# Kernel tuning notes

Hardware: AMD Instinct MI355X
Metric: run time of the kernel (lower is better)

The kernel has to match this reference:

```python
import jax, jax.numpy as jnp
import numpy as np

N_USERS = 100000
N_ITEMS = 100000
D_FEAT = 256
BATCH = 8192
CLASSES = 5
E = 500000
D_CONV = 128
D_RAW = 256
D_EMB = 256
NUM_BASIS = 2
BN_EPS = 1e-3  # tf.contrib.layers.batch_norm default epsilon


def _bn_params(key, dim):
    # packed [gamma, beta, moving_mean, moving_var]
    return jnp.stack([jnp.ones(dim), jnp.zeros(dim), jnp.zeros(dim), jnp.ones(dim)]).astype(jnp.float32)


def setup_inputs() -> dict:
    key = jax.random.key(0)
    ks = jax.random.split(key, 24)
    s = lambda fan_in, fan_out: np.sqrt(2.0 / (fan_in + fan_out)).astype(np.float32)
    inp = {
        'user_feat': jax.random.normal(ks[0], (N_USERS, D_FEAT), jnp.float32),
        'item_feat': jax.random.normal(ks[1], (N_ITEMS, D_FEAT), jnp.float32),
        'user_idx': jax.random.randint(ks[2], (BATCH,), 0, N_USERS, jnp.int32),
        'item_idx': jax.random.randint(ks[3], (BATCH,), 0, N_ITEMS, jnp.int32),
        'user_edge_src': jax.random.randint(ks[4], (CLASSES, E), 0, N_ITEMS, jnp.int32),
        'user_edge_dst': jax.random.randint(ks[5], (CLASSES, E), 0, BATCH, jnp.int32),
        'user_edge_w': jax.random.uniform(ks[6], (CLASSES, E), jnp.float32),
        'item_edge_src': jax.random.randint(ks[7], (CLASSES, E), 0, N_USERS, jnp.int32),
        'item_edge_dst': jax.random.randint(ks[8], (CLASSES, E), 0, BATCH, jnp.int32),
        'item_edge_w': jax.random.uniform(ks[9], (CLASSES, E), jnp.float32),
        'W_fu': jax.random.normal(ks[10], (D_FEAT, D_RAW), jnp.float32) * s(D_FEAT, D_RAW),
        'b_fu': jnp.zeros((D_RAW,), jnp.float32),
        'W_fi': jax.random.normal(ks[11], (D_FEAT, D_RAW), jnp.float32) * s(D_FEAT, D_RAW),
        'b_fi': jnp.zeros((D_RAW,), jnp.float32),
        'W_uc': jax.random.normal(ks[12], (CLASSES, D_FEAT, D_CONV), jnp.float32) * s(D_FEAT, D_CONV),
        'W_ic': jax.random.normal(ks[13], (CLASSES, D_FEAT, D_CONV), jnp.float32) * s(D_FEAT, D_CONV),
        'bn_fu': _bn_params(ks[14], D_RAW),
        'bn_hu': _bn_params(ks[15], CLASSES * D_CONV),
        'bn_fi': _bn_params(ks[16], D_RAW),
        'bn_hi': _bn_params(ks[17], CLASSES * D_CONV),
        'W2_fu': jax.random.normal(ks[18], (D_RAW, D_EMB), jnp.float32) * s(D_RAW, D_EMB),
        'W2_hu': jax.random.normal(ks[19], (CLASSES * D_CONV, D_EMB), jnp.float32) * s(CLASSES * D_CONV, D_EMB),
        'W2_fi': jax.random.normal(ks[20], (D_RAW, D_EMB), jnp.float32) * s(D_RAW, D_EMB),
        'W2_hi': jax.random.normal(ks[21], (CLASSES * D_CONV, D_EMB), jnp.float32) * s(CLASSES * D_CONV, D_EMB),
        'Wdec': jax.random.normal(ks[22], (NUM_BASIS, D_EMB, D_EMB), jnp.float32) * s(D_EMB, D_EMB),
        'Wcomb': jax.random.normal(ks[23], (CLASSES, NUM_BASIS), jnp.float32) * s(CLASSES, NUM_BASIS),
    }
    return inp


def _bn(x, p):
    gamma, beta, mean, var = p[0], p[1], p[2], p[3]
    return gamma * (x - mean) * jax.lax.rsqrt(var + BN_EPS) + beta


def _agg(feat, src, dst, w, n_rows):
    # weighted sparse [B, N] x dense [N, D] aggregation via gather + segment_sum
    msgs = feat[src] * w[:, None]  # [E, D]
    return jax.ops.segment_sum(msgs, dst, num_segments=n_rows)


def reference(user_feat, item_feat, user_idx, item_idx,
              user_edge_src, user_edge_dst, user_edge_w,
              item_edge_src, item_edge_dst, item_edge_w,
              W_fu, b_fu, W_fi, b_fi, W_uc, W_ic,
              bn_fu, bn_hu, bn_fi, bn_hi,
              W2_fu, W2_hu, W2_fi, W2_hi, Wdec, Wcomb):
    B = user_idx.shape[0]
    classes = W_uc.shape[0]

    # batch row selection (sparse.matmul with one-hot selector == gather)
    f_user = user_feat[user_idx] @ W_fu + b_fu  # [B, D_RAW]
    f_item = item_feat[item_idx] @ W_fi + b_fi

    # per-class graph convolution: aggregate opposite-side features, project, stack
    h_user = jnp.concatenate(
        [_agg(item_feat, user_edge_src[c], user_edge_dst[c], user_edge_w[c], B) @ W_uc[c]
         for c in range(classes)], axis=1)  # [B, classes*D_CONV]
    h_item = jnp.concatenate(
        [_agg(user_feat, item_edge_src[c], item_edge_dst[c], item_edge_w[c], B) @ W_ic[c]
         for c in range(classes)], axis=1)

    # batchnorm (inference stats) + relu  (dropout rate 0 -> identity)
    f_user = jax.nn.relu(_bn(f_user, bn_fu))
    f_item = jax.nn.relu(_bn(f_item, bn_fi))
    h_user = jax.nn.relu(_bn(h_user, bn_hu))
    h_item = jax.nn.relu(_bn(h_item, bn_hi))

    user_emb = jax.nn.relu(f_user @ W2_fu + h_user @ W2_hu)  # [B, D_EMB]
    item_emb = jax.nn.relu(f_item @ W2_fi + h_item @ W2_hi)

    # bilinear decoder: per-class kernel = sum_k Wcomb[r,k] * Wdec[k]
    kernels = jnp.einsum('rk,kij->rij', Wcomb, Wdec)  # [classes, D_EMB, D_EMB]
    logits = jnp.einsum('bi,rij,bj->br', user_emb, kernels, item_emb)  # [B, classes]
    return logits


if __name__ == '__main__':
    out = reference(**setup_inputs())
    print(out.shape, out.dtype)
```

## Files before the change

kernel.cpp:

```cpp
#include <hip/hip_runtime.h>
#include <cstdint>
#include <cstddef>

#define NBATCH   8192
#define DFEAT    256
#define DCONV    128
#define NCLASS   5
#define NEDGE    500000
#define NUSERS   100000
#define BN_EPS   1e-3f
#define NBUCKET  128
#define BROWS    64
#define CAP      4608
#define NPHB     16
#define NPHU     13

typedef unsigned short u16;
typedef short bf16x8_t __attribute__((ext_vector_type(8)));
typedef float f32x4_t  __attribute__((ext_vector_type(4)));

__device__ __forceinline__ u16 f2bf(float x) {
    unsigned u = __float_as_uint(x);
    u += 0x7FFF + ((u >> 16) & 1);
    return (u16)(u >> 16);
}
__device__ __forceinline__ float bf2f(u16 h) {
    return __uint_as_float(((unsigned)h) << 16);
}

template<int AF32>
__device__ __forceinline__ void mfma_tiles_t(
    const void* __restrict__ Av, int lda, const int* __restrict__ gather,
    const u16* __restrict__ BT, int K,
    int tileM, int tileN, u16* As, u16* Bs, f32x4_t acc[4])
{
    const int t    = threadIdx.x;
    const int rowi = t >> 2;
    const int kc   = t & 3;
    const int w    = t >> 6;
    const int lane = t & 63;

    int ar = gather ? gather[tileM + rowi] : (tileM + rowi);
    const u16*   Ap16 = (const u16*)Av   + (size_t)ar * lda + kc * 8;
    const float* Apf  = (const float*)Av + (size_t)ar * lda + kc * 8;
    const u16* Bp = BT + (size_t)(tileN + rowi) * K + kc * 8;
    u16* Aw = As + (size_t)(((rowi >> 4) * 64) + (rowi & 15) + 16 * kc) * 8;
    u16* Bw = Bs + (size_t)(((rowi >> 4) * 64) + (rowi & 15) + 16 * kc) * 8;
    const u16* Ar = As + (size_t)(w * 64 + lane) * 8;

    for (int k0 = 0; k0 < K; k0 += 32) {
        __syncthreads();
        if (AF32) {
            float4 a0 = *(const float4*)(Apf + k0);
            float4 a1 = *(const float4*)(Apf + k0 + 4);
            ushort4 p0, p1;
            p0.x = f2bf(a0.x); p0.y = f2bf(a0.y); p0.z = f2bf(a0.z); p0.w = f2bf(a0.w);
            p1.x = f2bf(a1.x); p1.y = f2bf(a1.y); p1.z = f2bf(a1.z); p1.w = f2bf(a1.w);
            *(ushort4*)Aw = p0;
            *(ushort4*)(Aw + 4) = p1;
        } else {
            *(uint4*)Aw = *(const uint4*)(Ap16 + k0);
        }
        *(uint4*)Bw = *(const uint4*)(Bp + k0);
        __syncthreads();
        bf16x8_t av = *(const bf16x8_t*)Ar;
        #pragma unroll
        for (int nb = 0; nb < 4; ++nb) {
            bf16x8_t bv = *(const bf16x8_t*)(Bs + (size_t)(nb * 64 + lane) * 8);
            acc[nb] = __builtin_amdgcn_mfma_f32_16x16x32_bf16(av, bv, acc[nb], 0, 0, 0);
        }
    }
}

__device__ __forceinline__ void epilogue(
    f32x4_t acc[4], int tileM, int tileN,
    const float* __restrict__ bias, const float* __restrict__ bn, int bn_ld,
    int relu, u16* __restrict__ out_bf, float* __restrict__ out_f32, int ldc)
{
    const int t = threadIdx.x, w = t >> 6, lane = t & 63;
    const int row0 = tileM + w * 16 + (lane >> 4) * 4;
    #pragma unroll
    for (int nb = 0; nb < 4; ++nb) {
        int col = tileN + nb * 16 + (lane & 15);
        float g = 1.f, be = 0.f, mu = 0.f, va = 1.f, bs = 0.f;
        if (bn)   { g = bn[col]; be = bn[bn_ld + col]; mu = bn[2 * bn_ld + col]; va = bn[3 * bn_ld + col]; }
        if (bias) bs = bias[col];
        #pragma unroll
        for (int r = 0; r < 4; ++r) {
            float x = acc[nb][r] + bs;
            if (bn)   x = g * (x - mu) * rsqrtf(va + BN_EPS) + be;
            if (relu) x = fmaxf(x, 0.f);
            size_t o = (size_t)(row0 + r) * ldc + col;
            if (out_bf) out_bf[o] = f2bf(x);
            else        out_f32[o] = x;
        }
    }
}

__global__ __launch_bounds__(256) void k_gemm_f(
    const float* __restrict__ uf, const float* __restrict__ itf,
    const int* __restrict__ uidx, const int* __restrict__ iidx,
    const u16* __restrict__ WTu, const u16* __restrict__ WTi,
    const float* __restrict__ bu, const float* __restrict__ bi,
    const float* __restrict__ bnu, const float* __restrict__ bni,
    u16* __restrict__ outu, u16* __restrict__ outi)
{
    __shared__ __align__(16) u16 As[2048], Bs[2048];
    f32x4_t z4 = {0.f, 0.f, 0.f, 0.f};
    f32x4_t acc[4] = {z4, z4, z4, z4};
    int z = blockIdx.z;
    const float* feat = z ? itf : uf;
    const int* idx  = z ? iidx : uidx;
    const u16* WT   = z ? WTi : WTu;
    const float* bias = z ? bi : bu;
    const float* bn   = z ? bni : bnu;
    u16* out = z ? outi : outu;
    int tileM = blockIdx.x * 64, tileN = blockIdx.y * 64;
    mfma_tiles_t<1>(feat, 256, idx, WT, 256, tileM, tileN, As, Bs, acc);
    epilogue(acc, tileM, tileN, bias, bn, 256, 1, out, nullptr, 256);
}

__global__ __launch_bounds__(256) void k_hproj(
    const u16* __restrict__ agg, const u16* __restrict__ WucT, const u16* __restrict__ WicT,
    const float* __restrict__ bn_hu, const float* __restrict__ bn_hi,
    u16* __restrict__ h_user, u16* __restrict__ h_item)
{
    __shared__ __align__(16) u16 As[2048], Bs[2048];
    f32x4_t z4 = {0.f, 0.f, 0.f, 0.f};
    f32x4_t acc[4] = {z4, z4, z4, z4};
    int cs = blockIdx.z, c = cs % NCLASS, side = cs / NCLASS;
    const u16* A  = agg + (size_t)cs * NBATCH * DFEAT;
    const u16* BT = (side ? WicT : WucT) + (size_t)c * DCONV * DFEAT;
    const float* bn = (side ? bn_hi : bn_hu) + c * DCONV;
    u16* out = (side ? h_item : h_user) + c * DCONV;
    int tileM = blockIdx.x * 64, tileN = blockIdx.y * 64;
    mfma_tiles_t<0>(A, 256, nullptr, BT, 256, tileM, tileN, As, Bs, acc);
    epilogue(acc, tileM, tileN, nullptr, bn, NCLASS * DCONV, 1, out, nullptr, NCLASS * DCONV);
}

__global__ __launch_bounds__(256) void k_emb(
    const u16* __restrict__ fu, const u16* __restrict__ fi,
    const u16* __restrict__ hu, const u16* __restrict__ hi,
    const u16* __restrict__ W2fTu, const u16* __restrict__ W2hTu,
    const u16* __restrict__ W2fTi, const u16* __restrict__ W2hTi,
    u16* __restrict__ embu, u16* __restrict__ embi)
{
    __shared__ __align__(16) u16 As[2048], Bs[2048];
    f32x4_t z4 = {0.f, 0.f, 0.f, 0.f};
    f32x4_t acc[4] = {z4, z4, z4, z4};
    int z = blockIdx.z;
    const u16* fbf  = z ? fi : fu;
    const u16* hbf  = z ? hi : hu;
    const u16* W2fT = z ? W2fTi : W2fTu;
    const u16* W2hT = z ? W2hTi : W2hTu;
    u16* emb = z ? embi : embu;
    int tileM = blockIdx.x * 64, tileN = blockIdx.y * 64;
    mfma_tiles_t<0>(fbf, 256, nullptr, W2fT, 256, tileM, tileN, As, Bs, acc);
    mfma_tiles_t<0>(hbf, NCLASS * DCONV, nullptr, W2hT, NCLASS * DCONV, tileM, tileN, As, Bs, acc);
    epilogue(acc, tileM, tileN, nullptr, nullptr, 0, 1, emb, nullptr, 256);
}

__global__ __launch_bounds__(256) void k_dec(
    const u16* __restrict__ emb, const u16* __restrict__ WdecT,
    float* __restrict__ t0, float* __restrict__ t1)
{
    __shared__ __align__(16) u16 As[2048], Bs[2048];
    f32x4_t z4 = {0.f, 0.f, 0.f, 0.f};
    f32x4_t acc[4] = {z4, z4, z4, z4};
    int zi = blockIdx.z;
    const u16* BT = WdecT + (size_t)zi * 256 * 256;
    float* out = zi ? t1 : t0;
    int tileM = blockIdx.x * 64, tileN = blockIdx.y * 64;
    mfma_tiles_t<0>(emb, 256, nullptr, BT, 256, tileM, tileN, As, Bs, acc);
    epilogue(acc, tileM, tileN, nullptr, nullptr, 0, 0, nullptr, out, 256);
}

__global__ __launch_bounds__(256) void cvt_feat(
    const float* __restrict__ uf, const float* __restrict__ itf,
    u16* __restrict__ ubf, u16* __restrict__ ibf)
{
    const size_t n4 = (size_t)NUSERS * DFEAT / 4;
    for (size_t i = (size_t)blockIdx.x * 256 + threadIdx.x; i < 2 * n4;
         i += (size_t)gridDim.x * 256) {
        bool u = i < n4;
        size_t j = u ? i : i - n4;
        float4 v = u ? ((const float4*)uf)[j] : ((const float4*)itf)[j];
        ushort4 o;
        o.x = f2bf(v.x); o.y = f2bf(v.y); o.z = f2bf(v.z); o.w = f2bf(v.w);
        ((ushort4*)(u ? ubf : ibf))[j] = o;
    }
}

#define OFF_WFU   0
#define OFF_WFI   65536
#define OFF_WUC   131072
#define OFF_WIC   294912
#define OFF_W2FU  458752
#define OFF_W2HU  524288
#define OFF_W2FI  688128
#define OFF_W2HI  753664
#define OFF_WDEC  917504

__global__ __launch_bounds__(256) void cvt_wt(
    const float* __restrict__ Wfu, const float* __restrict__ Wfi,
    const float* __restrict__ Wuc, const float* __restrict__ Wic,
    const float* __restrict__ W2fu, const float* __restrict__ W2hu,
    const float* __restrict__ W2fi, const float* __restrict__ W2hi,
    const float* __restrict__ Wdec, u16* __restrict__ wT)
{
    __shared__ float tile[32][33];
    const float* in; u16* out; int K, N, B;
    switch (blockIdx.y) {
        case 0: in = Wfu;  out = wT + OFF_WFU;  K = 256; N = 256; B = 1; break;
        case 1: in = Wfi;  out = wT + OFF_WFI;  K = 256; N = 256; B = 1; break;
        case 2: in = Wuc;  out = wT + OFF_WUC;  K = 256; N = 128; B = 5; break;
        case 3: in = Wic;  out = wT + OFF_WIC;  K = 256; N = 128; B = 5; break;
        case 4: in = W2fu; out = wT + OFF_W2FU; K = 256; N = 256; B = 1; break;
        case 5: in = W2hu; out = wT + OFF_W2HU; K = 640; N = 256; B = 1; break;
        case 6: in = W2fi; out = wT + OFF_W2FI; K = 256; N = 256; B = 1; break;
        case 7: in = W2hi; out = wT + OFF_W2HI; K = 640; N = 256; B = 1; break;
        default: in = Wdec; out = wT + OFF_WDEC; K = 256; N = 256; B = 2; break;
    }
    int tk = K >> 5, tn = N >> 5;
    int tid = blockIdx.x;
    if (tid >= B * tk * tn) return;
    int b  = tid / (tk * tn);
    int r  = tid - b * tk * tn;
    int kt = r % tk, nt = r / tk;
    int k0 = kt * 32, n0 = nt * 32;
    int ty = threadIdx.x >> 5, tx = threadIdx.x & 31;
    const float* ip = in + (size_t)b * K * N;
    u16* op = out + (size_t)b * N * K;
    #pragma unroll
    for (int i = 0; i < 4; ++i) {
        int row = ty + 8 * i;
        tile[row][tx] = ip[(size_t)(k0 + row) * N + (n0 + tx)];
    }
    __syncthreads();
    #pragma unroll
    for (int i = 0; i < 4; ++i) {
        int row = ty + 8 * i;
        op[(size_t)(n0 + row) * K + (k0 + tx)] = f2bf(tile[tx][row]);
    }
}

__global__ __launch_bounds__(256) void init_bcur(int* __restrict__ bcur)
{
    int i = blockIdx.x * 256 + threadIdx.x;
    if (i < 10 * NBUCKET) bcur[i] = (i & (NBUCKET - 1)) * CAP;
}

__global__ __launch_bounds__(256) void partition_kernel(
    const int* __restrict__ u_src, const int* __restrict__ u_dst, const float* __restrict__ u_w,
    const int* __restrict__ i_src, const int* __restrict__ i_dst, const float* __restrict__ i_w,
    int* __restrict__ bcur, uint2* __restrict__ part)
{
    __shared__ int hist[NBUCKET];
    __shared__ int cur[NBUCKET];
    int cs = blockIdx.y;
    const int* srcp; const int* dstp; const float* wp;
    if (cs < NCLASS) {
        srcp = u_src + (size_t)cs * NEDGE;
        dstp = u_dst + (size_t)cs * NEDGE;
        wp   = u_w   + (size_t)cs * NEDGE;
    } else {
        int c = cs - NCLASS;
        srcp = i_src + (size_t)c * NEDGE;
        dstp = i_dst + (size_t)c * NEDGE;
        wp   = i_w   + (size_t)c * NEDGE;
    }
    int lo_e = (int)(((long long)blockIdx.x * NEDGE) / gridDim.x);
    int hi_e = (int)(((long long)(blockIdx.x + 1) * NEDGE) / gridDim.x);

    for (int i = threadIdx.x; i < NBUCKET; i += 256) hist[i] = 0;
    __syncthreads();
    for (int e = lo_e + threadIdx.x; e < hi_e; e += 256)
        atomicAdd(&hist[dstp[e] >> 6], 1);
    __syncthreads();
    for (int i = threadIdx.x; i < NBUCKET; i += 256)
        cur[i] = atomicAdd(&bcur[cs * NBUCKET + i], hist[i]);
    __syncthreads();
    uint2* out = part + (size_t)cs * NBUCKET * CAP;
    for (int e = lo_e + threadIdx.x; e < hi_e; e += 256) {
        int dst = dstp[e];
        int bkt = dst >> 6;
        int pos = atomicAdd(&cur[bkt], 1);
        if (pos < bkt * CAP + CAP)
            out[pos] = make_uint2((unsigned)srcp[e] | ((unsigned)(dst & 63) << 24),
                                  __float_as_uint(wp[e]));
    }
}

__device__ __forceinline__ int edge_key(unsigned x) {
    return (int)((x >> 24) * NPHB) + (int)((x & 0xFFFFFFu) >> 13);
}

__global__ __launch_bounds__(512) void spmm_sorted(
    const u16* __restrict__ item_bf, const u16* __restrict__ user_bf,
    const uint2* __restrict__ part, const int* __restrict__ bcur,
    u16* __restrict__ agg)
{
    __shared__ int bin_cnt[BROWS * NPHB];
    __shared__ int bin_off[BROWS * NPHB + 1];
    __shared__ int bin_cur[BROWS * NPHB];
    __shared__ int wsum[8];
    __shared__ __align__(8) uint2 sorted[CAP];
    int id   = blockIdx.x;
    int side = id & 1;
    int k    = id >> 1;
    int c    = k >> 7;
    int b    = k & 127;
    int cs   = side * NCLASS + c;
    const u16* feat = side ? user_bf : item_bf;
    int n = bcur[cs * NBUCKET + b] - b * CAP;
    if (n > CAP) n = CAP;
    const uint2* ew = part + ((size_t)cs * NBUCKET + b) * CAP;
    int tid = threadIdx.x, wave = tid >> 6, lane = tid & 63;

    bin_cnt[tid] = 0;
    bin_cnt[tid + 512] = 0;
    __syncthreads();
    for (int e = tid; e < n; e += 512)
        atomicAdd(&bin_cnt[edge_key(ew[e].x)], 1);
    __syncthreads();
    {
        int i2 = tid * 2;
        int c0 = bin_cnt[i2], c1 = bin_cnt[i2 + 1];
        int s = c0 + c1;
        int v = s;
        #pragma unroll
        for (int o = 1; o < 64; o <<= 1) {
            int u = __shfl_up(v, o);
            if (lane >= o) v += u;
        }
        if (lane == 63) wsum[wave] = v;
        __syncthreads();
        if (tid < 8) {
            int s8 = wsum[tid];
            #pragma unroll
            for (int o = 1; o < 8; o <<= 1) {
                int u = __shfl_up(s8, o);
                if (lane >= o) s8 += u;
            }
            wsum[tid] = s8;
        }
        __syncthreads();
        int base = (wave ? wsum[wave - 1] : 0) + (v - s);
        bin_off[i2] = base;
        bin_off[i2 + 1] = base + c0;
        bin_cur[i2] = base;
        bin_cur[i2 + 1] = base + c0;
        if (tid == 511) bin_off[1024] = base + s;
    }
    __syncthreads();
    for (int e = tid; e < n; e += 512) {
        uint2 p = ew[e];
        int pos = atomicAdd(&bin_cur[edge_key(p.x)], 1);
        sorted[pos] = p;
    }
    __syncthreads();

    int rowbase = cs * NBATCH + b * BROWS;
    float ax[8], ay[8], az[8], aw[8];
    #pragma unroll
    for (int r0 = 0; r0 < 8; ++r0) { ax[r0] = 0.f; ay[r0] = 0.f; az[r0] = 0.f; aw[r0] = 0.f; }

    for (int ph = 0; ph < NPHU; ++ph) {
        #pragma unroll
        for (int r0 = 0; r0 < 8; ++r0) {
            int bi = (wave * 8 + r0) * NPHB + ph;
            int j0 = bin_off[bi], j1 = bin_off[bi + 1];
            int j = j0;
            for (; j + 7 < j1; j += 8) {
                uint2 p[8];
                #pragma unroll
                for (int q = 0; q < 8; ++q) p[q] = sorted[j + q];
                ushort4 v[8];
                #pragma unroll
                for (int q = 0; q < 8; ++q)
                    v[q] = *(const ushort4*)&feat[(size_t)(p[q].x & 0xFFFFFF) * DFEAT + lane * 4];
                #pragma unroll
                for (int q = 0; q < 8; ++q) {
                    float w = __uint_as_float(p[q].y);
                    ax[r0] += w * bf2f(v[q].x);
                    ay[r0] += w * bf2f(v[q].y);
                    az[r0] += w * bf2f(v[q].z);
                    aw[r0] += w * bf2f(v[q].w);
                }
            }
            for (; j + 3 < j1; j += 4) {
                uint2 p0 = sorted[j], p1 = sorted[j + 1], p2 = sorted[j + 2], p3 = sorted[j + 3];
                ushort4 v0 = *(const ushort4*)&feat[(size_t)(p0.x & 0xFFFFFF) * DFEAT + lane * 4];
                ushort4 v1 = *(const ushort4*)&feat[(size_t)(p1.x & 0xFFFFFF) * DFEAT + lane * 4];
                ushort4 v2 = *(const ushort4*)&feat[(size_t)(p2.x & 0xFFFFFF) * DFEAT + lane * 4];
                ushort4 v3 = *(const ushort4*)&feat[(size_t)(p3.x & 0xFFFFFF) * DFEAT + lane * 4];
                float w0 = __uint_as_float(p0.y), w1 = __uint_as_float(p1.y);
                float w2 = __uint_as_float(p2.y), w3 = __uint_as_float(p3.y);
                ax[r0] += w0 * bf2f(v0.x) + w1 * bf2f(v1.x) + w2 * bf2f(v2.x) + w3 * bf2f(v3.x);
                ay[r0] += w0 * bf2f(v0.y) + w1 * bf2f(v1.y) + w2 * bf2f(v2.y) + w3 * bf2f(v3.y);
                az[r0] += w0 * bf2f(v0.z) + w1 * bf2f(v1.z) + w2 * bf2f(v2.z) + w3 * bf2f(v3.z);
                aw[r0] += w0 * bf2f(v0.w) + w1 * bf2f(v1.w) + w2 * bf2f(v2.w) + w3 * bf2f(v3.w);
            }
            for (; j < j1; ++j) {
                uint2 p0 = sorted[j];
                ushort4 v0 = *(const ushort4*)&feat[(size_t)(p0.x & 0xFFFFFF) * DFEAT + lane * 4];
                float w0 = __uint_as_float(p0.y);
                ax[r0] += w0 * bf2f(v0.x);
                ay[r0] += w0 * bf2f(v0.y);
                az[r0] += w0 * bf2f(v0.z);
                aw[r0] += w0 * bf2f(v0.w);
            }
        }
    }

    #pragma unroll
    for (int r0 = 0; r0 < 8; ++r0) {
        ushort4 o4;
        o4.x = f2bf(ax[r0]); o4.y = f2bf(ay[r0]); o4.z = f2bf(az[r0]); o4.w = f2bf(aw[r0]);
        *(ushort4*)&agg[(size_t)(rowbase + wave * 8 + r0) * 256 + lane * 4] = o4;
    }
}

__global__ __launch_bounds__(256) void decoder_kernel(
    const float* __restrict__ t0, const float* __restrict__ t1,
    const u16* __restrict__ item_emb, const float* __restrict__ Wcomb,
    float* __restrict__ out)
{
    int wave = threadIdx.x >> 6;
    int lane = threadIdx.x & 63;
    int b = blockIdx.x * 4 + wave;
    const u16*   ie = item_emb + (size_t)b * 256;
    const float* p0 = t0 + (size_t)b * 256;
    const float* p1 = t1 + (size_t)b * 256;
    float s0 = 0.f, s1 = 0.f;
    #pragma unroll
    for (int j = lane; j < 256; j += 64) {
        float v = bf2f(ie[j]);
        s0 += p0[j] * v;
        s1 += p1[j] * v;
    }
    #pragma unroll
    for (int o = 32; o > 0; o >>= 1) {
        s0 += __shfl_down(s0, o);
        s1 += __shfl_down(s1, o);
    }
    if (lane == 0) {
        #pragma unroll
        for (int r = 0; r < NCLASS; ++r)
            out[b * NCLASS + r] = Wcomb[r * 2 + 0] * s0 + Wcomb[r * 2 + 1] * s1;
    }
}

extern "C" void kernel_launch(void* const* d_in, const int* in_sizes, int n_in,
                              void* d_out, int out_size, void* d_ws, size_t ws_size,
                              hipStream_t stream)
{
    const float* user_feat = (const float*)d_in[0];
    const float* item_feat = (const float*)d_in[1];
    const int*   user_idx  = (const int*)  d_in[2];
    const int*   item_idx  = (const int*)  d_in[3];
    const int*   u_src     = (const int*)  d_in[4];
    const int*   u_dst     = (const int*)  d_in[5];
    const float* u_w       = (const float*)d_in[6];
    const int*   i_src     = (const int*)  d_in[7];
    const int*   i_dst     = (const int*)  d_in[8];
    const float* i_w       = (const float*)d_in[9];
    const float* W_fu      = (const float*)d_in[10];
    const float* b_fu      = (const float*)d_in[11];
    const float* W_fi      = (const float*)d_in[12];
    const float* b_fi      = (const float*)d_in[13];
    const float* W_uc      = (const float*)d_in[14];
    const float* W_ic      = (const float*)d_in[15];
    const float* bn_fu     = (const float*)d_in[16];
    const float* bn_hu     = (const float*)d_in[17];
    const float* bn_fi     = (const float*)d_in[18];
    const float* bn_hi     = (const float*)d_in[19];
    const float* W2_fu     = (const float*)d_in[20];
    const float* W2_hu     = (const float*)d_in[21];
    const float* W2_fi     = (const float*)d_in[22];
    const float* W2_hi     = (const float*)d_in[23];
    const float* Wdec      = (const float*)d_in[24];
    const float* Wcomb     = (const float*)d_in[25];
    float* out = (float*)d_out;

    char* ws = (char*)d_ws;
    int*   bcur       = (int*)  (ws + 0);
    uint2* part_ew    = (uint2*)(ws + 65536);
    u16*   user_bf    = (u16*)  (ws + 47251456);
    u16*   item_bf    = (u16*)  (ws + 98451456);
    u16*   agg_bf     = (u16*)  (ws + 149651456);
    u16*   wT         = (u16*)  (ws + 191594496);
    u16*   f_user_bf  = (u16*)  (ws + 65536);
    u16*   f_item_bf  = (u16*)  (ws + 4259840);
    u16*   h_user_bf  = (u16*)  (ws + 8454144);
    u16*   h_item_bf  = (u16*)  (ws + 18939904);
    float* t0         = (float*)(ws + 149651456);
    float* t1         = (float*)(ws + 158040064);
    u16*   user_emb   = (u16*)  (ws + 166428672);
    u16*   item_emb   = (u16*)  (ws + 170622976);

    init_bcur<<<5, 256, 0, stream>>>(bcur);
    partition_kernel<<<dim3(128, 10), 256, 0, stream>>>(
        u_src, u_dst, u_w, i_src, i_dst, i_w, bcur, part_ew);

    cvt_feat<<<4096, 256, 0, stream>>>(user_feat, item_feat, user_bf, item_bf);
    cvt_wt<<<dim3(160, 9), 256, 0, stream>>>(W_fu, W_fi, W_uc, W_ic,
                                             W2_fu, W2_hu, W2_fi, W2_hi, Wdec, wT);

    spmm_sorted<<<dim3(2 * NCLASS * NBUCKET), 512, 0, stream>>>(
        item_bf, user_bf, part_ew, bcur, agg_bf);

    k_gemm_f<<<dim3(128, 4, 2), 256, 0, stream>>>(
        user_feat, item_feat, user_idx, item_idx, wT + OFF_WFU, wT + OFF_WFI,
        b_fu, b_fi, bn_fu, bn_fi, f_user_bf, f_item_bf);

    k_hproj<<<dim3(128, 2, 10), 256, 0, stream>>>(agg_bf, wT + OFF_WUC, wT + OFF_WIC,
                                                  bn_hu, bn_hi, h_user_bf, h_item_bf);

    k_emb<<<dim3(128, 4, 2), 256, 0, stream>>>(
        f_user_bf, f_item_bf, h_user_bf, h_item_bf,
        wT + OFF_W2FU, wT + OFF_W2HU, wT + OFF_W2FI, wT + OFF_W2HI,
        user_emb, item_emb);

    k_dec<<<dim3(128, 4, 2), 256, 0, stream>>>(user_emb, wT + OFF_WDEC, t0, t1);
    decoder_kernel<<<NBATCH / 4, 256, 0, stream>>>(t0, t1, item_emb, Wcomb, out);
}
```

Measured before the change: 710.2 us.

## Merge prep kernels and feature/hidden GEMMs into single launches; flatten spmm phase loop

```diff
diff --git a/kernel.cpp b/kernel.cpp
--- a/kernel.cpp
+++ b/kernel.cpp
@@ -97,45 +97,48 @@
     }
 }
 
-__global__ __launch_bounds__(256) void k_gemm_f(
+__global__ __launch_bounds__(256) void k_fh(
     const float* __restrict__ uf, const float* __restrict__ itf,
     const int* __restrict__ uidx, const int* __restrict__ iidx,
     const u16* __restrict__ WTu, const u16* __restrict__ WTi,
     const float* __restrict__ bu, const float* __restrict__ bi,
     const float* __restrict__ bnu, const float* __restrict__ bni,
-    u16* __restrict__ outu, u16* __restrict__ outi)
+    u16* __restrict__ outu, u16* __restrict__ outi,
+    const u16* __restrict__ agg, const u16* __restrict__ WucT, const u16* __restrict__ WicT,
+    const float* __restrict__ bn_hu, const float* __restrict__ bn_hi,
+    u16* __restrict__ h_user, u16* __restrict__ h_item)
 {
     __shared__ __align__(16) u16 As[2048], Bs[2048];
     f32x4_t z4 = {0.f, 0.f, 0.f, 0.f};
     f32x4_t acc[4] = {z4, z4, z4, z4};
-    int z = blockIdx.z;
-    const float* feat = z ? itf : uf;
-    const int* idx  = z ? iidx : uidx;
-    const u16* WT   = z ? WTi : WTu;
-    const float* bias = z ? bi : bu;
-    const float* bn   = z ? bni : bnu;
-    u16* out = z ? outi : outu;
-    int tileM = blockIdx.x * 64, tileN = blockIdx.y * 64;
-    mfma_tiles_t<1>(feat, 256, idx, WT, 256, tileM, tileN, As, Bs, acc);
-    epilogue(acc, tileM, tileN, bias, bn, 256, 1, out, nullptr, 256);
-}
-
-__global__ __launch_bounds__(256) void k_hproj(
-    const u16* __restrict__ agg, const u16* __restrict__ WucT, const u16* __restrict__ WicT,
-    const float* __restrict__ bn_hu, const float* __restrict__ bn_hi,
-    u16* __restrict__ h_user, u16* __restrict__ h_item)
-{
-    __shared__ __align__(16) u16 As[2048], Bs[2048];
-    f32x4_t z4 = {0.f, 0.f, 0.f, 0.f};
-    f32x4_t acc[4] = {z4, z4, z4, z4};
-    int cs = blockIdx.z, c = cs % NCLASS, side = cs / NCLASS;
-    const u16* A  = agg + (size_t)cs * NBATCH * DFEAT;
-    const u16* BT = (side ? WicT : WucT) + (size_t)c * DCONV * DFEAT;
-    const float* bn = (side ? bn_hi : bn_hu) + c * DCONV;
-    u16* out = (side ? h_item : h_user) + c * DCONV;
-    int tileM = blockIdx.x * 64, tileN = blockIdx.y * 64;
-    mfma_tiles_t<0>(A, 256, nullptr, BT, 256, tileM, tileN, As, Bs, acc);
-    epilogue(acc, tileM, tileN, nullptr, bn, NCLASS * DCONV, 1, out, nullptr, NCLASS * DCONV);
+    int id = blockIdx.x;
+    if (id < 1024) {
+        int z  = id >> 9;
+        int ny = (id >> 7) & 3;
+        int mx = id & 127;
+        const float* feat = z ? itf : uf;
+        const int* idx  = z ? iidx : uidx;
+        const u16* WT   = z ? WTi : WTu;
+        const float* bias = z ? bi : bu;
+        const float* bn   = z ? bni : bnu;
+        u16* out = z ? outi : outu;
+        int tileM = mx * 64, tileN = ny * 64;
+        mfma_tiles_t<1>(feat, 256, idx, WT, 256, tileM, tileN, As, Bs, acc);
+        epilogue(acc, tileM, tileN, bias, bn, 256, 1, out, nullptr, 256);
+    } else {
+        int r  = id - 1024;
+        int cs = r >> 8;
+        int ny = (r >> 7) & 1;
+        int mx = r & 127;
+        int c = cs % NCLASS, side = cs / NCLASS;
+        const u16* A  = agg + (size_t)cs * NBATCH * DFEAT;
+        const u16* BT = (side ? WicT : WucT) + (size_t)c * DCONV * DFEAT;
+        const float* bn = (side ? bn_hi : bn_hu) + c * DCONV;
+        u16* out = (side ? h_item : h_user) + c * DCONV;
+        int tileM = mx * 64, tileN = ny * 64;
+        mfma_tiles_t<0>(A, 256, nullptr, BT, 256, tileM, tileN, As, Bs, acc);
+        epilogue(acc, tileM, tileN, nullptr, bn, NCLASS * DCONV, 1, out, nullptr, NCLASS * DCONV);
+    }
 }
 
 __global__ __launch_bounds__(256) void k_emb(
@@ -175,22 +178,6 @@
     epilogue(acc, tileM, tileN, nullptr, nullptr, 0, 0, nullptr, out, 256);
 }
 
-__global__ __launch_bounds__(256) void cvt_feat(
-    const float* __restrict__ uf, const float* __restrict__ itf,
-    u16* __restrict__ ubf, u16* __restrict__ ibf)
-{
-    const size_t n4 = (size_t)NUSERS * DFEAT / 4;
-    for (size_t i = (size_t)blockIdx.x * 256 + threadIdx.x; i < 2 * n4;
-         i += (size_t)gridDim.x * 256) {
-        bool u = i < n4;
-        size_t j = u ? i : i - n4;
-        float4 v = u ? ((const float4*)uf)[j] : ((const float4*)itf)[j];
-        ushort4 o;
-        o.x = f2bf(v.x); o.y = f2bf(v.y); o.z = f2bf(v.z); o.w = f2bf(v.w);
-        ((ushort4*)(u ? ubf : ibf))[j] = o;
-    }
-}
-
 #define OFF_WFU   0
 #define OFF_WFI   65536
 #define OFF_WUC   131072
@@ -201,46 +188,105 @@
 #define OFF_W2HI  753664
 #define OFF_WDEC  917504
 
-__global__ __launch_bounds__(256) void cvt_wt(
+__global__ __launch_bounds__(256) void prep_all(
+    const int* __restrict__ u_src, const int* __restrict__ u_dst, const float* __restrict__ u_w,
+    const int* __restrict__ i_src, const int* __restrict__ i_dst, const float* __restrict__ i_w,
+    int* __restrict__ bcur, uint2* __restrict__ part,
+    const float* __restrict__ uf, const float* __restrict__ itf,
+    u16* __restrict__ ubf, u16* __restrict__ ibf,
     const float* __restrict__ Wfu, const float* __restrict__ Wfi,
     const float* __restrict__ Wuc, const float* __restrict__ Wic,
     const float* __restrict__ W2fu, const float* __restrict__ W2hu,
     const float* __restrict__ W2fi, const float* __restrict__ W2hi,
     const float* __restrict__ Wdec, u16* __restrict__ wT)
 {
-    __shared__ float tile[32][33];
-    const float* in; u16* out; int K, N, B;
-    switch (blockIdx.y) {
-        case 0: in = Wfu;  out = wT + OFF_WFU;  K = 256; N = 256; B = 1; break;
-        case 1: in = Wfi;  out = wT + OFF_WFI;  K = 256; N = 256; B = 1; break;
-        case 2: in = Wuc;  out = wT + OFF_WUC;  K = 256; N = 128; B = 5; break;
-        case 3: in = Wic;  out = wT + OFF_WIC;  K = 256; N = 128; B = 5; break;
-        case 4: in = W2fu; out = wT + OFF_W2FU; K = 256; N = 256; B = 1; break;
-        case 5: in = W2hu; out = wT + OFF_W2HU; K = 640; N = 256; B = 1; break;
-        case 6: in = W2fi; out = wT + OFF_W2FI; K = 256; N = 256; B = 1; break;
-        case 7: in = W2hi; out = wT + OFF_W2HI; K = 640; N = 256; B = 1; break;
-        default: in = Wdec; out = wT + OFF_WDEC; K = 256; N = 256; B = 2; break;
-    }
-    int tk = K >> 5, tn = N >> 5;
-    int tid = blockIdx.x;
-    if (tid >= B * tk * tn) return;
-    int b  = tid / (tk * tn);
-    int r  = tid - b * tk * tn;
-    int kt = r % tk, nt = r / tk;
-    int k0 = kt * 32, n0 = nt * 32;
-    int ty = threadIdx.x >> 5, tx = threadIdx.x & 31;
-    const float* ip = in + (size_t)b * K * N;
-    u16* op = out + (size_t)b * N * K;
-    #pragma unroll
-    for (int i = 0; i < 4; ++i) {
-        int row = ty + 8 * i;
-        tile[row][tx] = ip[(size_t)(k0 + row) * N + (n0 + tx)];
-    }
-    __syncthreads();
-    #pragma unroll
-    for (int i = 0; i < 4; ++i) {
-        int row = ty + 8 * i;
-        op[(size_t)(n0 + row) * K + (k0 + tx)] = f2bf(tile[tx][row]);
+    __shared__ union {
+        struct { int hist[NBUCKET]; int cur[NBUCKET]; } p;
+        float tile[32][33];
+    } sm;
+    int id = blockIdx.x;
+    if (id < 1280) {
+        int cs = id / 128;
+        int bx = id - cs * 128;
+        const int* srcp; const int* dstp; const float* wp;
+        if (cs < NCLASS) {
+            srcp = u_src + (size_t)cs * NEDGE;
+            dstp = u_dst + (size_t)cs * NEDGE;
+            wp   = u_w   + (size_t)cs * NEDGE;
+        } else {
+            int c = cs - NCLASS;
+            srcp = i_src + (size_t)c * NEDGE;
+            dstp = i_dst + (size_t)c * NEDGE;
+            wp   = i_w   + (size_t)c * NEDGE;
+        }
+        int lo_e = (int)(((long long)bx * NEDGE) >> 7);
+        int hi_e = (int)(((long long)(bx + 1) * NEDGE) >> 7);
+
+        for (int i = threadIdx.x; i < NBUCKET; i += 256) sm.p.hist[i] = 0;
+        __syncthreads();
+        for (int e = lo_e + threadIdx.x; e < hi_e; e += 256)
+            atomicAdd(&sm.p.hist[dstp[e] >> 6], 1);
+        __syncthreads();
+        for (int i = threadIdx.x; i < NBUCKET; i += 256)
+            sm.p.cur[i] = atomicAdd(&bcur[cs * NBUCKET + i], sm.p.hist[i]);
+        __syncthreads();
+        uint2* out = part + (size_t)cs * NBUCKET * CAP;
+        for (int e = lo_e + threadIdx.x; e < hi_e; e += 256) {
+            int dst = dstp[e];
+            int bkt = dst >> 6;
+            int pos = atomicAdd(&sm.p.cur[bkt], 1);
+            if (pos < bkt * CAP + CAP)
+                out[pos] = make_uint2((unsigned)srcp[e] | ((unsigned)(dst & 63) << 24),
+                                      __float_as_uint(wp[e]));
+        }
+    } else if (id < 1280 + 4096) {
+        int bx = id - 1280;
+        const size_t n4 = (size_t)NUSERS * DFEAT / 4;
+        for (size_t i = (size_t)bx * 256 + threadIdx.x; i < 2 * n4;
+             i += (size_t)4096 * 256) {
+            bool u = i < n4;
+            size_t j = u ? i : i - n4;
+            float4 v = u ? ((const float4*)uf)[j] : ((const float4*)itf)[j];
+            ushort4 o;
+            o.x = f2bf(v.x); o.y = f2bf(v.y); o.z = f2bf(v.z); o.w = f2bf(v.w);
+            ((ushort4*)(u ? ubf : ibf))[j] = o;
+        }
+    } else {
+        int r0 = id - (1280 + 4096);
+        int cse = r0 / 160;
+        int tid = r0 - cse * 160;
+        const float* in; u16* out; int K, N, B;
+        switch (cse) {
+            case 0: in = Wfu;  out = wT + OFF_WFU;  K = 256; N = 256; B = 1; break;
+            case 1: in = Wfi;  out = wT + OFF_WFI;  K = 256; N = 256; B = 1; break;
+            case 2: in = Wuc;  out = wT + OFF_WUC;  K = 256; N = 128; B = 5; break;
+            case 3: in = Wic;  out = wT + OFF_WIC;  K = 256; N = 128; B = 5; break;
+            case 4: in = W2fu; out = wT + OFF_W2FU; K = 256; N = 256; B = 1; break;
+            case 5: in = W2hu; out = wT + OFF_W2HU; K = 640; N = 256; B = 1; break;
+            case 6: in = W2fi; out = wT + OFF_W2FI; K = 256; N = 256; B = 1; break;
+            case 7: in = W2hi; out = wT + OFF_W2HI; K = 640; N = 256; B = 1; break;
+            default: in = Wdec; out = wT + OFF_WDEC; K = 256; N = 256; B = 2; break;
+        }
+        int tk = K >> 5, tn = N >> 5;
+        if (tid >= B * tk * tn) return;
+        int b  = tid / (tk * tn);
+        int r  = tid - b * tk * tn;
+        int kt = r % tk, nt = r / tk;
+        int k0 = kt * 32, n0 = nt * 32;
+        int ty = threadIdx.x >> 5, tx = threadIdx.x & 31;
+        const float* ip = in + (size_t)b * K * N;
+        u16* op = out + (size_t)b * N * K;
+        #pragma unroll
+        for (int i = 0; i < 4; ++i) {
+            int row = ty + 8 * i;
+            sm.tile[row][tx] = ip[(size_t)(k0 + row) * N + (n0 + tx)];
+        }
+        __syncthreads();
+        #pragma unroll
+        for (int i = 0; i < 4; ++i) {
+            int row = ty + 8 * i;
+            op[(size_t)(n0 + row) * K + (k0 + tx)] = f2bf(sm.tile[tx][row]);
+        }
     }
 }
 
@@ -248,47 +294,6 @@
 {
     int i = blockIdx.x * 256 + threadIdx.x;
     if (i < 10 * NBUCKET) bcur[i] = (i & (NBUCKET - 1)) * CAP;
-}
-
-__global__ __launch_bounds__(256) void partition_kernel(
-    const int* __restrict__ u_src, const int* __restrict__ u_dst, const float* __restrict__ u_w,
-    const int* __restrict__ i_src, const int* __restrict__ i_dst, const float* __restrict__ i_w,
-    int* __restrict__ bcur, uint2* __restrict__ part)
-{
-    __shared__ int hist[NBUCKET];
-    __shared__ int cur[NBUCKET];
-    int cs = blockIdx.y;
-    const int* srcp; const int* dstp; const float* wp;
-    if (cs < NCLASS) {
-        srcp = u_src + (size_t)cs * NEDGE;
-        dstp = u_dst + (size_t)cs * NEDGE;
-        wp   = u_w   + (size_t)cs * NEDGE;
-    } else {
-        int c = cs - NCLASS;
-        srcp = i_src + (size_t)c * NEDGE;
-        dstp = i_dst + (size_t)c * NEDGE;
-        wp   = i_w   + (size_t)c * NEDGE;
-    }
-    int lo_e = (int)(((long long)blockIdx.x * NEDGE) / gridDim.x);
-    int hi_e = (int)(((long long)(blockIdx.x + 1) * NEDGE) / gridDim.x);
-
-    for (int i = threadIdx.x; i < NBUCKET; i += 256) hist[i] = 0;
-    __syncthreads();
-    for (int e = lo_e + threadIdx.x; e < hi_e; e += 256)
-        atomicAdd(&hist[dstp[e] >> 6], 1);
-    __syncthreads();
-    for (int i = threadIdx.x; i < NBUCKET; i += 256)
-        cur[i] = atomicAdd(&bcur[cs * NBUCKET + i], hist[i]);
-    __syncthreads();
-    uint2* out = part + (size_t)cs * NBUCKET * CAP;
-    for (int e = lo_e + threadIdx.x; e < hi_e; e += 256) {
-        int dst = dstp[e];
-        int bkt = dst >> 6;
-        int pos = atomicAdd(&cur[bkt], 1);
-        if (pos < bkt * CAP + CAP)
-            out[pos] = make_uint2((unsigned)srcp[e] | ((unsigned)(dst & 63) << 24),
-                                  __float_as_uint(wp[e]));
-    }
 }
 
 __device__ __forceinline__ int edge_key(unsigned x) {
@@ -365,51 +370,49 @@
     #pragma unroll
     for (int r0 = 0; r0 < 8; ++r0) { ax[r0] = 0.f; ay[r0] = 0.f; az[r0] = 0.f; aw[r0] = 0.f; }
 
-    for (int ph = 0; ph < NPHU; ++ph) {
-        #pragma unroll
-        for (int r0 = 0; r0 < 8; ++r0) {
-            int bi = (wave * 8 + r0) * NPHB + ph;
-            int j0 = bin_off[bi], j1 = bin_off[bi + 1];
-            int j = j0;
-            for (; j + 7 < j1; j += 8) {
-                uint2 p[8];
-                #pragma unroll
-                for (int q = 0; q < 8; ++q) p[q] = sorted[j + q];
-                ushort4 v[8];
-                #pragma unroll
-                for (int q = 0; q < 8; ++q)
-                    v[q] = *(const ushort4*)&feat[(size_t)(p[q].x & 0xFFFFFF) * DFEAT + lane * 4];
-                #pragma unroll
-                for (int q = 0; q < 8; ++q) {
-                    float w = __uint_as_float(p[q].y);
-                    ax[r0] += w * bf2f(v[q].x);
-                    ay[r0] += w * bf2f(v[q].y);
-                    az[r0] += w * bf2f(v[q].z);
-                    aw[r0] += w * bf2f(v[q].w);
-                }
+    #pragma unroll
+    for (int r0 = 0; r0 < 8; ++r0) {
+        int base = (wave * 8 + r0) * NPHB;
+        int j0 = bin_off[base], j1 = bin_off[base + NPHU];
+        int j = j0;
+        for (; j + 7 < j1; j += 8) {
+            uint2 p[8];
+            #pragma unroll
+            for (int q = 0; q < 8; ++q) p[q] = sorted[j + q];
+            ushort4 v[8];
+            #pragma unroll
+            for (int q = 0; q < 8; ++q)
+                v[q] = *(const ushort4*)&feat[(size_t)(p[q].x & 0xFFFFFF) * DFEAT + lane * 4];
+            #pragma unroll
+            for (int q = 0; q < 8; ++q) {
+                float w = __uint_as_float(p[q].y);
+                ax[r0] += w * bf2f(v[q].x);
+                ay[r0] += w * bf2f(v[q].y);
+                az[r0] += w * bf2f(v[q].z);
+                aw[r0] += w * bf2f(v[q].w);
             }
-            for (; j + 3 < j1; j += 4) {
-                uint2 p0 = sorted[j], p1 = sorted[j + 1], p2 = sorted[j + 2], p3 = sorted[j + 3];
-                ushort4 v0 = *(const ushort4*)&feat[(size_t)(p0.x & 0xFFFFFF) * DFEAT + lane * 4];
-                ushort4 v1 = *(const ushort4*)&feat[(size_t)(p1.x & 0xFFFFFF) * DFEAT + lane * 4];
-                ushort4 v2 = *(const ushort4*)&feat[(size_t)(p2.x & 0xFFFFFF) * DFEAT + lane * 4];
-                ushort4 v3 = *(const ushort4*)&feat[(size_t)(p3.x & 0xFFFFFF) * DFEAT + lane * 4];
-                float w0 = __uint_as_float(p0.y), w1 = __uint_as_float(p1.y);
-                float w2 = __uint_as_float(p2.y), w3 = __uint_as_float(p3.y);
-                ax[r0] += w0 * bf2f(v0.x) + w1 * bf2f(v1.x) + w2 * bf2f(v2.x) + w3 * bf2f(v3.x);
-                ay[r0] += w0 * bf2f(v0.y) + w1 * bf2f(v1.y) + w2 * bf2f(v2.y) + w3 * bf2f(v3.y);
-                az[r0] += w0 * bf2f(v0.z) + w1 * bf2f(v1.z) + w2 * bf2f(v2.z) + w3 * bf2f(v3.z);
-                aw[r0] += w0 * bf2f(v0.w) + w1 * bf2f(v1.w) + w2 * bf2f(v2.w) + w3 * bf2f(v3.w);
-            }
-            for (; j < j1; ++j) {
-                uint2 p0 = sorted[j];
-                ushort4 v0 = *(const ushort4*)&feat[(size_t)(p0.x & 0xFFFFFF) * DFEAT + lane * 4];
-                float w0 = __uint_as_float(p0.y);
-                ax[r0] += w0 * bf2f(v0.x);
-                ay[r0] += w0 * bf2f(v0.y);
-                az[r0] += w0 * bf2f(v0.z);
-                aw[r0] += w0 * bf2f(v0.w);
-            }
+        }
+        for (; j + 3 < j1; j += 4) {
+            uint2 p0 = sorted[j], p1 = sorted[j + 1], p2 = sorted[j + 2], p3 = sorted[j + 3];
+            ushort4 v0 = *(const ushort4*)&feat[(size_t)(p0.x & 0xFFFFFF) * DFEAT + lane * 4];
+            ushort4 v1 = *(const ushort4*)&feat[(size_t)(p1.x & 0xFFFFFF) * DFEAT + lane * 4];
+            ushort4 v2 = *(const ushort4*)&feat[(size_t)(p2.x & 0xFFFFFF) * DFEAT + lane * 4];
+            ushort4 v3 = *(const ushort4*)&feat[(size_t)(p3.x & 0xFFFFFF) * DFEAT + lane * 4];
+            float w0 = __uint_as_float(p0.y), w1 = __uint_as_float(p1.y);
+            float w2 = __uint_as_float(p2.y), w3 = __uint_as_float(p3.y);
+            ax[r0] += w0 * bf2f(v0.x) + w1 * bf2f(v1.x) + w2 * bf2f(v2.x) + w3 * bf2f(v3.x);
+            ay[r0] += w0 * bf2f(v0.y) + w1 * bf2f(v1.y) + w2 * bf2f(v2.y) + w3 * bf2f(v3.y);
+            az[r0] += w0 * bf2f(v0.z) + w1 * bf2f(v1.z) + w2 * bf2f(v2.z) + w3 * bf2f(v3.z);
+            aw[r0] += w0 * bf2f(v0.w) + w1 * bf2f(v1.w) + w2 * bf2f(v2.w) + w3 * bf2f(v3.w);
+        }
+        for (; j < j1; ++j) {
+            uint2 p0 = sorted[j];
+            ushort4 v0 = *(const ushort4*)&feat[(size_t)(p0.x & 0xFFFFFF) * DFEAT + lane * 4];
+            float w0 = __uint_as_float(p0.y);
+            ax[r0] += w0 * bf2f(v0.x);
+            ay[r0] += w0 * bf2f(v0.y);
+            az[r0] += w0 * bf2f(v0.z);
+            aw[r0] += w0 * bf2f(v0.w);
         }
     }
 
@@ -500,22 +503,18 @@
     u16*   item_emb   = (u16*)  (ws + 170622976);
 
     init_bcur<<<5, 256, 0, stream>>>(bcur);
-    partition_kernel<<<dim3(128, 10), 256, 0, stream>>>(
-        u_src, u_dst, u_w, i_src, i_dst, i_w, bcur, part_ew);
-
-    cvt_feat<<<4096, 256, 0, stream>>>(user_feat, item_feat, user_bf, item_bf);
-    cvt_wt<<<dim3(160, 9), 256, 0, stream>>>(W_fu, W_fi, W_uc, W_ic,
-                                             W2_fu, W2_hu, W2_fi, W2_hi, Wdec, wT);
+    prep_all<<<6816, 256, 0, stream>>>(
+        u_src, u_dst, u_w, i_src, i_dst, i_w, bcur, part_ew,
+        user_feat, item_feat, user_bf, item_bf,
+        W_fu, W_fi, W_uc, W_ic, W2_fu, W2_hu, W2_fi, W2_hi, Wdec, wT);
 
     spmm_sorted<<<dim3(2 * NCLASS * NBUCKET), 512, 0, stream>>>(
         item_bf, user_bf, part_ew, bcur, agg_bf);
 
-    k_gemm_f<<<dim3(128, 4, 2), 256, 0, stream>>>(
+    k_fh<<<3584, 256, 0, stream>>>(
         user_feat, item_feat, user_idx, item_idx, wT + OFF_WFU, wT + OFF_WFI,
-        b_fu, b_fi, bn_fu, bn_fi, f_user_bf, f_item_bf);
-
-    k_hproj<<<dim3(128, 2, 10), 256, 0, stream>>>(agg_bf, wT + OFF_WUC, wT + OFF_WIC,
-                                                  bn_hu, bn_hi, h_user_bf, h_item_bf);
+        b_fu, b_fi, bn_fu, bn_fi, f_user_bf, f_item_bf,
+        agg_bf, wT + OFF_WUC, wT + OFF_WIC, bn_hu, bn_hi, h_user_bf, h_item_bf);
 
     k_emb<<<dim3(128, 4, 2), 256, 0, stream>>>(
         f_user_bf, f_item_bf, h_user_bf, h_item_bf,
```

After: 762.5 us. 1.07x slower.
